# Optimization experiments

Hardware: AMD Instinct MI355X
Metric: run time of the kernel (lower is better)

## Reference

```python
import jax, jax.numpy as jnp
import numpy as np

N = 100_000   # nodes
E = 1_600_000 # edges (avg degree 16)
D_IN = 128
D_H = 128
PROP_STEP = 2


def setup_inputs() -> dict:
    key = jax.random.key(0)
    k = jax.random.split(key, 6)
    in_feat = jax.random.normal(k[0], (N, D_IN), dtype=jnp.float32)
    edge_index = jax.random.randint(k[1], (2, E), 0, N, dtype=jnp.int64)
    s1 = 1.0 / np.sqrt(D_IN)
    s2 = 1.0 / np.sqrt(D_H)
    W1 = jax.random.normal(k[2], (D_IN, D_H), dtype=jnp.float32) * s1
    b1 = jnp.zeros((D_H,), dtype=jnp.float32)
    W2 = jax.random.normal(k[3], (D_H, D_H), dtype=jnp.float32) * s2
    b2 = jnp.zeros((D_H,), dtype=jnp.float32)
    return {"in_feat": in_feat, "edge_index": edge_index,
            "W1": W1, "b1": b1, "W2": W2, "b2": b2}


def _degree_norms(src, dst):
    ones = jnp.ones((src.shape[0],), dtype=jnp.float32)
    deg_out = jax.ops.segment_sum(ones, src, num_segments=N)
    deg_in = jax.ops.segment_sum(ones, dst, num_segments=N)
    # DGL clamps degree to >= 1 before norm='both'
    dout = jnp.maximum(deg_out, 1.0) ** -0.5  # applied to source features
    din = jnp.maximum(deg_in, 1.0) ** -0.5    # applied after aggregation
    return dout, din


def _gcn_conv(x, src, dst, dout, din, W, b):
    # D_in^{-1/2} A D_out^{-1/2} X W + b  (DGL GraphConv, norm='both')
    m = (x * dout[:, None])[src]                      # [E, D] gather
    agg = jax.ops.segment_sum(m, dst, num_segments=N) # [N, D] scatter-add
    return (agg * din[:, None]) @ W + b


def reference(in_feat, edge_index, W1, b1, W2, b2):
    src, dst = edge_index[0], edge_index[1]
    dout, din = _degree_norms(src, dst)
    h = _gcn_conv(in_feat, src, dst, dout, din, W1, b1)
    for _ in range(1, PROP_STEP):
        # relu=False and eval mode -> no relu / dropout
        h = _gcn_conv(h, src, dst, dout, din, W2, b2)
    return h
```

## Files before the change

### kernel.cpp

```cpp
#include <hip/hip_runtime.h>
#include <cstdint>
#include <cstddef>

#define DF 128
#define PB 512
#define RSH 8
#define RNG 256
#define CAP 6144

typedef short bf16x8 __attribute__((ext_vector_type(8)));
typedef float f32x4 __attribute__((ext_vector_type(4)));

__device__ __forceinline__ unsigned short f2b(float f) {
  unsigned u = __builtin_bit_cast(unsigned, f);
  u = (u + 0x7FFFu + ((u >> 16) & 1u)) >> 16;
  return (unsigned short)u;
}
__device__ __forceinline__ float b2f(unsigned short h) {
  return __builtin_bit_cast(float, (unsigned)h << 16);
}
__device__ __forceinline__ unsigned pack2(float lo, float hi) {
  return (unsigned)f2b(lo) | ((unsigned)f2b(hi) << 16);
}

__device__ __forceinline__ int edge_at(const void* ei, long long idx, int is32) {
  return is32 ? ((const int*)ei)[idx] : (int)((const long long*)ei)[idx];
}

__global__ void detect_dtype_kernel(const unsigned* __restrict__ ei, long long nelem,
                                    int* __restrict__ flag) {
  long long half = nelem / 2;
  int t = threadIdx.x + blockIdx.x * blockDim.x;
  long long step = (half + 2047) / 2048;
  long long k = (long long)t * step;
  if (k < half && ei[2 * k + 1] != 0) atomicOr(flag, 1);
}

__global__ __launch_bounds__(256) void part_count_kernel(
    const void* __restrict__ ei, long long E, int nbuck, int chunk,
    int* __restrict__ H, const int* __restrict__ flag) {
  __shared__ int hd[512], hs[512];
  int is32 = *flag;
  int blk = blockIdx.x, t = threadIdx.x;
  for (int i = t; i < 512; i += 256) { hd[i] = 0; hs[i] = 0; }
  __syncthreads();
  long long lo = (long long)blk * chunk;
  long long hi = lo + chunk; if (hi > E) hi = E;
  for (long long e = lo + t; e < hi; e += 256) {
    int s = edge_at(ei, e, is32);
    int d = edge_at(ei, E + e, is32);
    atomicAdd(&hs[s >> RSH], 1);
    atomicAdd(&hd[d >> RSH], 1);
  }
  __syncthreads();
  for (int b = t; b < nbuck; b += 256) {
    H[(size_t)b * PB + blk] = hd[b];
    H[((size_t)nbuck + b) * PB + blk] = hs[b];
  }
}

__device__ __forceinline__ int wave_incl_scan(int v, int lane) {
#pragma unroll
  for (int off = 1; off < 64; off <<= 1) {
    int t = __shfl_up(v, off, 64);
    if (lane >= off) v += t;
  }
  return v;
}

__global__ void chunk_sum_kernel(const int* __restrict__ deg, int* __restrict__ partials, int n) {
  __shared__ int wsum[16];
  int tid = threadIdx.x, lane = tid & 63, wid = tid >> 6;
  int base = blockIdx.x * 4096 + tid * 4;
  int s = 0;
#pragma unroll
  for (int q = 0; q < 4; ++q) { int i = base + q; if (i < n) s += deg[i]; }
#pragma unroll
  for (int off = 32; off; off >>= 1) s += __shfl_down(s, off, 64);
  if (lane == 0) wsum[wid] = s;
  __syncthreads();
  if (tid == 0) {
    int t = 0;
#pragma unroll
    for (int w = 0; w < 16; ++w) t += wsum[w];
    partials[blockIdx.x] = t;
  }
}

__global__ void scan_partials_kernel(int* __restrict__ partials, int nb) {
  int lane = threadIdx.x;
  int carry = 0;
  for (int base = 0; base < nb; base += 64) {
    int i = base + lane;
    int v = (i < nb) ? partials[i] : 0;
    int s = wave_incl_scan(v, lane);
    if (i < nb) partials[i] = s - v + carry;
    carry += __shfl(s, 63, 64);
  }
}

__global__ void scan_chunk_kernel(const int* __restrict__ deg, const int* __restrict__ chunk_off,
                                  int* __restrict__ row_ptr, int n) {
  __shared__ int wsum[16];
  int tid = threadIdx.x, lane = tid & 63, wid = tid >> 6;
  int base = blockIdx.x * 4096 + tid * 4;
  int v0 = (base + 0 < n) ? deg[base + 0] : 0;
  int v1 = (base + 1 < n) ? deg[base + 1] : 0;
  int v2 = (base + 2 < n) ? deg[base + 2] : 0;
  int v3 = (base + 3 < n) ? deg[base + 3] : 0;
  int p0 = v0, p1 = p0 + v1, p2 = p1 + v2, p3 = p2 + v3;
  int ws = wave_incl_scan(p3, lane);
  if (lane == 63) wsum[wid] = ws;
  __syncthreads();
  if (wid == 0) {
    int x = (lane < 16) ? wsum[lane] : 0;
    x = wave_incl_scan(x, lane);
    if (lane < 16) wsum[lane] = x;
  }
  __syncthreads();
  int off = (wid > 0 ? wsum[wid - 1] : 0) + (ws - p3) + chunk_off[blockIdx.x];
  if (base + 0 < n) row_ptr[base + 1] = off + p0;
  if (base + 1 < n) row_ptr[base + 2] = off + p1;
  if (base + 2 < n) row_ptr[base + 3] = off + p2;
  if (base + 3 < n) row_ptr[base + 4] = off + p3;
  if (blockIdx.x == 0 && tid == 0) row_ptr[0] = 0;
}

__global__ __launch_bounds__(256) void part_scatter_kernel(
    const void* __restrict__ ei, long long E, int nbuck, int chunk,
    const int* __restrict__ Hs, unsigned* __restrict__ pack_d,
    unsigned char* __restrict__ src_loc, const int* __restrict__ flag) {
  __shared__ int hd[512], hs[512], bd[512], bs[512];
  int is32 = *flag;
  int blk = blockIdx.x, t = threadIdx.x;
  for (int i = t; i < 512; i += 256) { hd[i] = 0; hs[i] = 0; }
  __syncthreads();
  for (int b = t; b < nbuck; b += 256) {
    bd[b] = Hs[(size_t)b * PB + blk];
    bs[b] = Hs[((size_t)nbuck + b) * PB + blk] - (int)E;
  }
  __syncthreads();
  long long lo = (long long)blk * chunk;
  long long hi = lo + chunk; if (hi > E) hi = E;
  for (long long e = lo + t; e < hi; e += 256) {
    int s = edge_at(ei, e, is32);
    int d = edge_at(ei, E + e, is32);
    int kb = d >> RSH;
    int rd = atomicAdd(&hd[kb], 1);
    pack_d[bd[kb] + rd] = ((unsigned)(d & (RNG - 1)) << 24) | (unsigned)s;
    int ks = s >> RSH;
    int rs = atomicAdd(&hs[ks], 1);
    src_loc[bs[ks] + rs] = (unsigned char)(s & (RNG - 1));
  }
}

__global__ __launch_bounds__(256) void bucket_build_kernel(
    const unsigned* __restrict__ pack_d, const int* __restrict__ Hs,
    long long E, int n, int* __restrict__ row_ptr, float* __restrict__ nin,
    int* __restrict__ csr_src) {
  __shared__ unsigned stage[CAP];
  __shared__ int cnt[RNG], cur[RNG], woff[4];
  int b = blockIdx.x, t = threadIdx.x;
  int lane = t & 63, wv = t >> 6;
  int start = Hs[(size_t)b * PB];
  int end = Hs[(size_t)(b + 1) * PB];
  int len = end - start;
  cnt[t] = 0;
  __syncthreads();
  bool fits = (len <= CAP);
  for (int i = t; i < len; i += 256) {
    unsigned p = pack_d[start + i];
    if (fits) stage[i] = p;
    atomicAdd(&cnt[p >> 24], 1);
  }
  __syncthreads();
  int dreg = cnt[t];
  int isc = wave_incl_scan(dreg, lane);
  if (lane == 63) woff[wv] = isc;
  __syncthreads();
  int add = 0;
#pragma unroll
  for (int w = 0; w < 4; ++w) if (w < wv) add += woff[w];
  int excl = isc - dreg + add;
  int nd = b * RNG + t;
  if (nd < n) {
    row_ptr[nd] = start + excl;
    nin[nd] = rsqrtf((float)(dreg > 1 ? dreg : 1));
  }
  if (b == (int)gridDim.x - 1 && t == 0) row_ptr[n] = (int)E;
  cur[t] = excl;
  __syncthreads();
  for (int i = t; i < len; i += 256) {
    unsigned p = fits ? stage[i] : pack_d[start + i];
    int dl = (int)(p >> 24);
    int r = atomicAdd(&cur[dl], 1);
    csr_src[start + r] = (int)(p & 0xFFFFFFu);
  }
}

__global__ __launch_bounds__(256) void src_deg_kernel(
    const unsigned char* __restrict__ src_loc, const int* __restrict__ Hs,
    int nbuck, long long E, int n, float* __restrict__ nout) {
  __shared__ int cnt[RNG];
  int b = blockIdx.x, t = threadIdx.x;
  int start = Hs[(size_t)(nbuck + b) * PB] - (int)E;
  int end = Hs[(size_t)(nbuck + b + 1) * PB] - (int)E;
  cnt[t] = 0;
  __syncthreads();
  for (int i = start + t; i < end; i += 256) atomicAdd(&cnt[src_loc[i]], 1);
  __syncthreads();
  int nd = b * RNG + t;
  if (nd < n) nout[nd] = rsqrtf((float)(cnt[t] > 1 ? cnt[t] : 1));
}

__global__ __launch_bounds__(256) void prescale_kernel(
    const float* __restrict__ x, const float* __restrict__ nout,
    unsigned short* __restrict__ xh, int n) {
  long long base = ((long long)blockIdx.x * 256 + threadIdx.x) * 8;
  if (base >= (long long)n * DF) return;
  float s = nout[(int)(base >> 7)];
  float4 a = *((const float4*)(x + base));
  float4 b = *((const float4*)(x + base + 4));
  uint4 o;
  o.x = pack2(a.x * s, a.y * s);
  o.y = pack2(a.z * s, a.w * s);
  o.z = pack2(b.x * s, b.y * s);
  o.w = pack2(b.z * s, b.w * s);
  *((uint4*)(xh + base)) = o;
}

__global__ void w_prep_kernel(const float* __restrict__ W1, const float* __restrict__ W2,
                              unsigned short* __restrict__ Wswz) {
  int chunk = blockIdx.x * 256 + threadIdx.x;
  if (chunk >= 8192) return;
  int w = chunk >> 12;
  int rem = chunk & 4095;
  int part = rem >> 11;
  int t = (rem >> 6) & 31;
  int l = rem & 63;
  int jb = t >> 2, ks = t & 3;
  const float* W = w ? W2 : W1;
  int c = jb * 16 + (l & 15);
  int k0 = ks * 32 + ((l >> 4) << 3);
  unsigned v[4];
#pragma unroll
  for (int p = 0; p < 4; ++p) {
    float f0 = W[(size_t)(k0 + 2 * p) * DF + c];
    float f1 = W[(size_t)(k0 + 2 * p + 1) * DF + c];
    unsigned short h0 = f2b(f0), h1 = f2b(f1);
    unsigned short o0 = part ? f2b(f0 - b2f(h0)) : h0;
    unsigned short o1 = part ? f2b(f1 - b2f(h1)) : h1;
    v[p] = (unsigned)o0 | ((unsigned)o1 << 16);
  }
  uint4 o; o.x = v[0]; o.y = v[1]; o.z = v[2]; o.w = v[3];
  ((uint4*)Wswz)[chunk] = o;
}

__global__ __launch_bounds__(256) void aggregate_bf16_kernel(
    const unsigned short* __restrict__ xh, const int* __restrict__ row_ptr,
    const int* __restrict__ csr_src, unsigned short* __restrict__ aggh, int n) {
  int wave = blockIdx.x * (blockDim.x >> 6) + (threadIdx.x >> 6);
  int lane = threadIdx.x & 63;
  if (wave >= n) return;
  int beg = row_ptr[wave], end = row_ptr[wave + 1];
  int deg = end - beg;
  int half = lane >> 5;
  int sub = lane & 31;
  float ax = 0.f, ay = 0.f, az = 0.f, aw = 0.f;
  for (int j0 = 0; j0 < deg; j0 += 64) {
    int li = beg + j0 + lane;
    int idx = csr_src[li < end ? li : (end - 1)];
    int cnt = deg - j0; if (cnt > 64) cnt = 64;
    int tfull = (cnt >> 4) << 3;
    for (int t0 = 0; t0 < tfull; t0 += 8) {
      ushort4 v[8];
#pragma unroll
      for (int u = 0; u < 8; ++u) {
        int s = __shfl(idx, 2 * (t0 + u) + half, 64);
        v[u] = *((const ushort4*)(xh + (size_t)s * DF) + sub);
      }
#pragma unroll
      for (int u = 0; u < 8; ++u) {
        ax += b2f(v[u].x); ay += b2f(v[u].y);
        az += b2f(v[u].z); aw += b2f(v[u].w);
      }
    }
    int cnt2 = (cnt + 1) >> 1;
    for (int t = tfull; t < cnt2; ++t) {
      int p = 2 * t + half;
      int s = __shfl(idx, p, 64);
      float m = (p < cnt) ? 1.f : 0.f;
      ushort4 v = *((const ushort4*)(xh + (size_t)s * DF) + sub);
      ax += b2f(v.x) * m; ay += b2f(v.y) * m;
      az += b2f(v.z) * m; aw += b2f(v.w) * m;
    }
  }
  ax += __shfl_down(ax, 32, 64);
  ay += __shfl_down(ay, 32, 64);
  az += __shfl_down(az, 32, 64);
  aw += __shfl_down(aw, 32, 64);
  if (half == 0) {
    uint2 pk; pk.x = pack2(ax, ay); pk.y = pack2(az, aw);
    *((uint2*)(aggh + (size_t)wave * DF + sub * 4)) = pk;
  }
}

template <int BF16OUT>
__global__ __launch_bounds__(256) void transform_mfma_kernel(
    const unsigned short* __restrict__ aggh, const unsigned short* __restrict__ Wswz,
    const float* __restrict__ nin, const float* __restrict__ bias,
    const float* __restrict__ sc_out, void* __restrict__ outp, int n, int ntiles) {
  __shared__ uint4 Wl[4096];
  int tid = threadIdx.x;
  for (int i = tid; i < 4096; i += 256) Wl[i] = ((const uint4*)Wswz)[i];
  __syncthreads();
  int l = tid & 63, wv = tid >> 6;
  int lr = l & 15, lg = l >> 4;
  for (int tile = blockIdx.x; tile < ntiles; tile += gridDim.x) {
    int rowbase = tile * 64 + wv * 16;
    int r_eff = rowbase + lr; if (r_eff > n - 1) r_eff = n - 1;
    const unsigned short* arow = aggh + (size_t)r_eff * DF + (lg << 3);
    bf16x8 a0 = *(const bf16x8*)(arow);
    bf16x8 a1 = *(const bf16x8*)(arow + 32);
    bf16x8 a2 = *(const bf16x8*)(arow + 64);
    bf16x8 a3 = *(const bf16x8*)(arow + 96);
    f32x4 acc[8];
#pragma unroll
    for (int jb = 0; jb < 8; ++jb) acc[jb] = (f32x4){0.f, 0.f, 0.f, 0.f};
#pragma unroll
    for (int ks = 0; ks < 4; ++ks) {
      bf16x8 a = (ks == 0) ? a0 : (ks == 1) ? a1 : (ks == 2) ? a2 : a3;
#pragma unroll
      for (int jb = 0; jb < 8; ++jb) {
        bf16x8 bh = *(const bf16x8*)&Wl[(jb * 4 + ks) * 64 + l];
        acc[jb] = __builtin_amdgcn_mfma_f32_16x16x32_bf16(a, bh, acc[jb], 0, 0, 0);
        bf16x8 bl = *(const bf16x8*)&Wl[2048 + (jb * 4 + ks) * 64 + l];
        acc[jb] = __builtin_amdgcn_mfma_f32_16x16x32_bf16(a, bl, acc[jb], 0, 0, 0);
      }
    }
    float ninq[4], soq[4];
#pragma unroll
    for (int q = 0; q < 4; ++q) {
      int r = rowbase + lg * 4 + q;
      ninq[q] = (r < n) ? nin[r] : 0.f;
      soq[q] = (r < n) ? (sc_out ? sc_out[r] : 1.f) : 0.f;
    }
#pragma unroll
    for (int jb = 0; jb < 8; ++jb) {
      int c = jb * 16 + lr;
      float bj = bias[c];
#pragma unroll
      for (int q = 0; q < 4; ++q) {
        int r = rowbase + lg * 4 + q;
        if (r < n) {
          float val = (acc[jb][q] * ninq[q] + bj) * soq[q];
          if (BF16OUT) {
            ((unsigned short*)outp)[(size_t)r * DF + c] = f2b(val);
          } else {
            ((float*)outp)[(size_t)r * DF + c] = val;
          }
        }
      }
    }
  }
}

extern "C" void kernel_launch(void* const* d_in, const int* in_sizes, int n_in,
                              void* d_out, int out_size, void* d_ws, size_t ws_size,
                              hipStream_t stream) {
  const float* in_feat = (const float*)d_in[0];
  const void*  ei      = d_in[1];
  const float* W1 = (const float*)d_in[2];
  const float* b1 = (const float*)d_in[3];
  const float* W2 = (const float*)d_in[4];
  const float* b2 = (const float*)d_in[5];
  float* out = (float*)d_out;

  const int N = in_sizes[0] / DF;
  const long long E = in_sizes[1] / 2;
  const int nbuck = (N + RNG - 1) >> RSH;
  const int M = 2 * nbuck * PB;
  const int NB2 = (M + 4095) / 4096;
  const int chunk = (int)((E + PB - 1) / PB);
  const int ntiles = (N + 63) / 64;

  size_t off = 0;
  auto take = [&](size_t nb) -> char* {
    char* p = (char*)d_ws + off;
    off += (nb + 255) & ~(size_t)255;
    return p;
  };
  int* H          = (int*)take((size_t)M * 4);
  int* Hs         = (int*)take((size_t)(M + 1) * 4);
  int* partials   = (int*)take((size_t)NB2 * 4);
  int* row_ptr    = (int*)take((size_t)(N + 1) * 4);
  float* nout     = (float*)take((size_t)N * 4);
  float* nin      = (float*)take((size_t)N * 4);
  int* flag       = (int*)take(4);
  unsigned* pack_d = (unsigned*)take((size_t)E * 4);
  unsigned char* src_loc = (unsigned char*)take((size_t)E);
  int* csr_src    = (int*)take((size_t)E * 4);
  unsigned short* x1h = (unsigned short*)take((size_t)N * DF * 2);
  unsigned short* h1h = (unsigned short*)take((size_t)N * DF * 2);
  unsigned short* aggh = (unsigned short*)take((size_t)N * DF * 2);
  unsigned short* Wswz = (unsigned short*)take(2 * 65536);
  (void)ws_size; (void)n_in; (void)out_size;

  hipMemsetAsync(flag, 0, 4, stream);
  detect_dtype_kernel<<<8, 256, 0, stream>>>((const unsigned*)ei, (long long)in_sizes[1], flag);

  part_count_kernel<<<PB, 256, 0, stream>>>(ei, E, nbuck, chunk, H, flag);
  chunk_sum_kernel<<<NB2, 1024, 0, stream>>>(H, partials, M);
  scan_partials_kernel<<<1, 64, 0, stream>>>(partials, NB2);
  scan_chunk_kernel<<<NB2, 1024, 0, stream>>>(H, partials, Hs, M);
  part_scatter_kernel<<<PB, 256, 0, stream>>>(ei, E, nbuck, chunk, Hs, pack_d, src_loc, flag);
  bucket_build_kernel<<<nbuck, 256, 0, stream>>>(pack_d, Hs, E, N, row_ptr, nin, csr_src);
  src_deg_kernel<<<nbuck, 256, 0, stream>>>(src_loc, Hs, nbuck, E, N, nout);

  w_prep_kernel<<<32, 256, 0, stream>>>(W1, W2, Wswz);

  int pb = (int)(((long long)N * DF / 8 + 255) / 256);
  prescale_kernel<<<pb, 256, 0, stream>>>(in_feat, nout, x1h, N);

  int ab = (N + 3) / 4;
  aggregate_bf16_kernel<<<ab, 256, 0, stream>>>(x1h, row_ptr, csr_src, aggh, N);
  transform_mfma_kernel<1><<<512, 256, 0, stream>>>(aggh, Wswz, nin, b1, nout, h1h, N, ntiles);
  aggregate_bf16_kernel<<<ab, 256, 0, stream>>>(h1h, row_ptr, csr_src, aggh, N);
  transform_mfma_kernel<0><<<512, 256, 0, stream>>>(aggh, Wswz + 32768, nin, b2, nullptr, out, N, ntiles);
}
```

Measured before the change: 313.1 us.

## Fuse aggregation with MFMA transform via per-wave LDS stripes and dynamic scheduling

Merges the gather/scatter aggregation and the MFMA linear transform into one persistent kernel. Each wave atomically grabs 16-node chunks, aggregates them into an LDS stripe and applies the weight matmul directly, so the intermediate aggregation buffer never goes through global memory. Also folds dtype detection into the partition kernels and source-degree counting into bucket_build, removing several launches. The trade-offs are a 512-block persistent grid with one wave per chunk, which may lower the memory-level parallelism of the gather, plus extra LDS pressure from the stripes alongside the weight tile.

Result: slower. 512.8 us (+63.8%).

```diff
diff --git a/kernel.cpp b/kernel.cpp
--- a/kernel.cpp
+++ b/kernel.cpp
@@ -27,25 +27,29 @@
   return is32 ? ((const int*)ei)[idx] : (int)((const long long*)ei)[idx];
 }
 
-__global__ void detect_dtype_kernel(const unsigned* __restrict__ ei, long long nelem,
-                                    int* __restrict__ flag) {
-  long long half = nelem / 2;
-  int t = threadIdx.x + blockIdx.x * blockDim.x;
-  long long step = (half + 2047) / 2048;
-  long long k = (long long)t * step;
-  if (k < half && ei[2 * k + 1] != 0) atomicOr(flag, 1);
+__device__ __forceinline__ int detect_is32(const void* ei, long long lo, long long hi,
+                                           int* s_flag) {
+  int t = threadIdx.x;
+  if (t == 0) *s_flag = 0;
+  __syncthreads();
+  int bad = 0;
+  long long cap = lo + 2048; if (cap > hi) cap = hi;
+  for (long long e = lo + t; e < cap; e += 256)
+    bad |= (((const unsigned*)ei)[2 * e + 1] != 0);
+  if (bad) atomicOr(s_flag, 1);
+  __syncthreads();
+  return *s_flag;
 }
 
 __global__ __launch_bounds__(256) void part_count_kernel(
     const void* __restrict__ ei, long long E, int nbuck, int chunk,
-    int* __restrict__ H, const int* __restrict__ flag) {
-  __shared__ int hd[512], hs[512];
-  int is32 = *flag;
+    int* __restrict__ H) {
+  __shared__ int hd[512], hs[512], s_flag;
   int blk = blockIdx.x, t = threadIdx.x;
   for (int i = t; i < 512; i += 256) { hd[i] = 0; hs[i] = 0; }
-  __syncthreads();
   long long lo = (long long)blk * chunk;
   long long hi = lo + chunk; if (hi > E) hi = E;
+  int is32 = detect_is32(ei, lo, hi, &s_flag);
   for (long long e = lo + t; e < hi; e += 256) {
     int s = edge_at(ei, e, is32);
     int d = edge_at(ei, E + e, is32);
@@ -129,19 +133,18 @@
 __global__ __launch_bounds__(256) void part_scatter_kernel(
     const void* __restrict__ ei, long long E, int nbuck, int chunk,
     const int* __restrict__ Hs, unsigned* __restrict__ pack_d,
-    unsigned char* __restrict__ src_loc, const int* __restrict__ flag) {
+    unsigned char* __restrict__ src_loc) {
   __shared__ int hd[512], hs[512], bd[512], bs[512];
-  int is32 = *flag;
+  __shared__ int s_flag;
   int blk = blockIdx.x, t = threadIdx.x;
   for (int i = t; i < 512; i += 256) { hd[i] = 0; hs[i] = 0; }
-  __syncthreads();
   for (int b = t; b < nbuck; b += 256) {
     bd[b] = Hs[(size_t)b * PB + blk];
     bs[b] = Hs[((size_t)nbuck + b) * PB + blk] - (int)E;
   }
-  __syncthreads();
   long long lo = (long long)blk * chunk;
   long long hi = lo + chunk; if (hi > E) hi = E;
+  int is32 = detect_is32(ei, lo, hi, &s_flag);
   for (long long e = lo + t; e < hi; e += 256) {
     int s = edge_at(ei, e, is32);
     int d = edge_at(ei, E + e, is32);
@@ -155,8 +158,9 @@
 }
 
 __global__ __launch_bounds__(256) void bucket_build_kernel(
-    const unsigned* __restrict__ pack_d, const int* __restrict__ Hs,
-    long long E, int n, int* __restrict__ row_ptr, float* __restrict__ nin,
+    const unsigned* __restrict__ pack_d, const unsigned char* __restrict__ src_loc,
+    const int* __restrict__ Hs, int nbuck, long long E, int n,
+    int* __restrict__ row_ptr, float* __restrict__ nin, float* __restrict__ nout,
     int* __restrict__ csr_src) {
   __shared__ unsigned stage[CAP];
   __shared__ int cnt[RNG], cur[RNG], woff[4];
@@ -196,20 +200,13 @@
     int r = atomicAdd(&cur[dl], 1);
     csr_src[start + r] = (int)(p & 0xFFFFFFu);
   }
-}
-
-__global__ __launch_bounds__(256) void src_deg_kernel(
-    const unsigned char* __restrict__ src_loc, const int* __restrict__ Hs,
-    int nbuck, long long E, int n, float* __restrict__ nout) {
-  __shared__ int cnt[RNG];
-  int b = blockIdx.x, t = threadIdx.x;
-  int start = Hs[(size_t)(nbuck + b) * PB] - (int)E;
-  int end = Hs[(size_t)(nbuck + b + 1) * PB] - (int)E;
+  __syncthreads();
   cnt[t] = 0;
   __syncthreads();
-  for (int i = start + t; i < end; i += 256) atomicAdd(&cnt[src_loc[i]], 1);
-  __syncthreads();
-  int nd = b * RNG + t;
+  int sstart = Hs[(size_t)(nbuck + b) * PB] - (int)E;
+  int send = Hs[(size_t)(nbuck + b + 1) * PB] - (int)E;
+  for (int i = sstart + t; i < send; i += 256) atomicAdd(&cnt[src_loc[i]], 1);
+  __syncthreads();
   if (nd < n) nout[nd] = rsqrtf((float)(cnt[t] > 1 ? cnt[t] : 1));
 }
 
@@ -256,74 +253,76 @@
   ((uint4*)Wswz)[chunk] = o;
 }
 
-__global__ __launch_bounds__(256) void aggregate_bf16_kernel(
+template <int BF16OUT>
+__global__ __launch_bounds__(256) void fused_conv_kernel(
     const unsigned short* __restrict__ xh, const int* __restrict__ row_ptr,
-    const int* __restrict__ csr_src, unsigned short* __restrict__ aggh, int n) {
-  int wave = blockIdx.x * (blockDim.x >> 6) + (threadIdx.x >> 6);
-  int lane = threadIdx.x & 63;
-  if (wave >= n) return;
-  int beg = row_ptr[wave], end = row_ptr[wave + 1];
-  int deg = end - beg;
-  int half = lane >> 5;
-  int sub = lane & 31;
-  float ax = 0.f, ay = 0.f, az = 0.f, aw = 0.f;
-  for (int j0 = 0; j0 < deg; j0 += 64) {
-    int li = beg + j0 + lane;
-    int idx = csr_src[li < end ? li : (end - 1)];
-    int cnt = deg - j0; if (cnt > 64) cnt = 64;
-    int tfull = (cnt >> 4) << 3;
-    for (int t0 = 0; t0 < tfull; t0 += 8) {
-      ushort4 v[8];
-#pragma unroll
-      for (int u = 0; u < 8; ++u) {
-        int s = __shfl(idx, 2 * (t0 + u) + half, 64);
-        v[u] = *((const ushort4*)(xh + (size_t)s * DF) + sub);
+    const int* __restrict__ csr_src, const unsigned short* __restrict__ Wswz,
+    const float* __restrict__ nin, const float* __restrict__ bias,
+    const float* __restrict__ sc_out, void* __restrict__ outp, int n,
+    int nchunks, int* __restrict__ ctr) {
+  __shared__ uint4 Wl[4096];
+  __shared__ unsigned short stripe[4][2048];
+  int tid = threadIdx.x;
+  for (int i = tid; i < 4096; i += 256) Wl[i] = ((const uint4*)Wswz)[i];
+  __syncthreads();
+  int l = tid & 63, wv = tid >> 6;
+  int half = l >> 5, sub = l & 31;
+  int lr = l & 15, lg = l >> 4;
+  unsigned short* st = stripe[wv];
+  for (;;) {
+    int chunk = 0;
+    if (l == 0) chunk = atomicAdd(ctr, 1);
+    chunk = __shfl(chunk, 0, 64);
+    if (chunk >= nchunks) break;
+    int base = chunk * 16;
+    for (int j = 0; j < 16; ++j) {
+      int node = base + j;
+      float ax = 0.f, ay = 0.f, az = 0.f, aw = 0.f;
+      if (node < n) {
+        int beg = row_ptr[node], end = row_ptr[node + 1];
+        int deg = end - beg;
+        for (int j0 = 0; j0 < deg; j0 += 64) {
+          int li = beg + j0 + l;
+          int idx = csr_src[li < end ? li : (end - 1)];
+          int cnt = deg - j0; if (cnt > 64) cnt = 64;
+          int tfull = (cnt >> 4) << 3;
+          for (int t0 = 0; t0 < tfull; t0 += 8) {
+            ushort4 v[8];
+#pragma unroll
+            for (int u = 0; u < 8; ++u) {
+              int s = __shfl(idx, 2 * (t0 + u) + half, 64);
+              v[u] = *((const ushort4*)(xh + (size_t)s * DF) + sub);
+            }
+#pragma unroll
+            for (int u = 0; u < 8; ++u) {
+              ax += b2f(v[u].x); ay += b2f(v[u].y);
+              az += b2f(v[u].z); aw += b2f(v[u].w);
+            }
+          }
+          int cnt2 = (cnt + 1) >> 1;
+          for (int t = tfull; t < cnt2; ++t) {
+            int p = 2 * t + half;
+            int s = __shfl(idx, p, 64);
+            float m = (p < cnt) ? 1.f : 0.f;
+            ushort4 v = *((const ushort4*)(xh + (size_t)s * DF) + sub);
+            ax += b2f(v.x) * m; ay += b2f(v.y) * m;
+            az += b2f(v.z) * m; aw += b2f(v.w) * m;
+          }
+        }
       }
-#pragma unroll
-      for (int u = 0; u < 8; ++u) {
-        ax += b2f(v[u].x); ay += b2f(v[u].y);
-        az += b2f(v[u].z); aw += b2f(v[u].w);
+      ax += __shfl_down(ax, 32, 64);
+      ay += __shfl_down(ay, 32, 64);
+      az += __shfl_down(az, 32, 64);
+      aw += __shfl_down(aw, 32, 64);
+      if (half == 0) {
+        uint2 pk; pk.x = pack2(ax, ay); pk.y = pack2(az, aw);
+        *((uint2*)(st + j * 128 + sub * 4)) = pk;
       }
     }
-    int cnt2 = (cnt + 1) >> 1;
-    for (int t = tfull; t < cnt2; ++t) {
-      int p = 2 * t + half;
-      int s = __shfl(idx, p, 64);
-      float m = (p < cnt) ? 1.f : 0.f;
-      ushort4 v = *((const ushort4*)(xh + (size_t)s * DF) + sub);
-      ax += b2f(v.x) * m; ay += b2f(v.y) * m;
-      az += b2f(v.z) * m; aw += b2f(v.w) * m;
-    }
-  }
-  ax += __shfl_down(ax, 32, 64);
-  ay += __shfl_down(ay, 32, 64);
-  az += __shfl_down(az, 32, 64);
-  aw += __shfl_down(aw, 32, 64);
-  if (half == 0) {
-    uint2 pk; pk.x = pack2(ax, ay); pk.y = pack2(az, aw);
-    *((uint2*)(aggh + (size_t)wave * DF + sub * 4)) = pk;
-  }
-}
-
-template <int BF16OUT>
-__global__ __launch_bounds__(256) void transform_mfma_kernel(
-    const unsigned short* __restrict__ aggh, const unsigned short* __restrict__ Wswz,
-    const float* __restrict__ nin, const float* __restrict__ bias,
-    const float* __restrict__ sc_out, void* __restrict__ outp, int n, int ntiles) {
-  __shared__ uint4 Wl[4096];
-  int tid = threadIdx.x;
-  for (int i = tid; i < 4096; i += 256) Wl[i] = ((const uint4*)Wswz)[i];
-  __syncthreads();
-  int l = tid & 63, wv = tid >> 6;
-  int lr = l & 15, lg = l >> 4;
-  for (int tile = blockIdx.x; tile < ntiles; tile += gridDim.x) {
-    int rowbase = tile * 64 + wv * 16;
-    int r_eff = rowbase + lr; if (r_eff > n - 1) r_eff = n - 1;
-    const unsigned short* arow = aggh + (size_t)r_eff * DF + (lg << 3);
-    bf16x8 a0 = *(const bf16x8*)(arow);
-    bf16x8 a1 = *(const bf16x8*)(arow + 32);
-    bf16x8 a2 = *(const bf16x8*)(arow + 64);
-    bf16x8 a3 = *(const bf16x8*)(arow + 96);
+    bf16x8 a0 = *(const bf16x8*)(st + lr * 128 + 0 * 32 + lg * 8);
+    bf16x8 a1 = *(const bf16x8*)(st + lr * 128 + 1 * 32 + lg * 8);
+    bf16x8 a2 = *(const bf16x8*)(st + lr * 128 + 2 * 32 + lg * 8);
+    bf16x8 a3 = *(const bf16x8*)(st + lr * 128 + 3 * 32 + lg * 8);
     f32x4 acc[8];
 #pragma unroll
     for (int jb = 0; jb < 8; ++jb) acc[jb] = (f32x4){0.f, 0.f, 0.f, 0.f};
@@ -341,7 +340,7 @@
     float ninq[4], soq[4];
 #pragma unroll
     for (int q = 0; q < 4; ++q) {
-      int r = rowbase + lg * 4 + q;
+      int r = base + lg * 4 + q;
       ninq[q] = (r < n) ? nin[r] : 0.f;
       soq[q] = (r < n) ? (sc_out ? sc_out[r] : 1.f) : 0.f;
     }
@@ -351,7 +350,7 @@
       float bj = bias[c];
 #pragma unroll
       for (int q = 0; q < 4; ++q) {
-        int r = rowbase + lg * 4 + q;
+        int r = base + lg * 4 + q;
         if (r < n) {
           float val = (acc[jb][q] * ninq[q] + bj) * soq[q];
           if (BF16OUT) {
@@ -382,7 +381,7 @@
   const int M = 2 * nbuck * PB;
   const int NB2 = (M + 4095) / 4096;
   const int chunk = (int)((E + PB - 1) / PB);
-  const int ntiles = (N + 63) / 64;
+  const int nchunks = (N + 15) / 16;
 
   size_t off = 0;
   auto take = [&](size_t nb) -> char* {
@@ -396,35 +395,32 @@
   int* row_ptr    = (int*)take((size_t)(N + 1) * 4);
   float* nout     = (float*)take((size_t)N * 4);
   float* nin      = (float*)take((size_t)N * 4);
-  int* flag       = (int*)take(4);
+  int* ctr        = (int*)take(8);
   unsigned* pack_d = (unsigned*)take((size_t)E * 4);
   unsigned char* src_loc = (unsigned char*)take((size_t)E);
   int* csr_src    = (int*)take((size_t)E * 4);
   unsigned short* x1h = (unsigned short*)take((size_t)N * DF * 2);
   unsigned short* h1h = (unsigned short*)take((size_t)N * DF * 2);
-  unsigned short* aggh = (unsigned short*)take((size_t)N * DF * 2);
   unsigned short* Wswz = (unsigned short*)take(2 * 65536);
   (void)ws_size; (void)n_in; (void)out_size;
 
-  hipMemsetAsync(flag, 0, 4, stream);
-  detect_dtype_kernel<<<8, 256, 0, stream>>>((const unsigned*)ei, (long long)in_sizes[1], flag);
-
-  part_count_kernel<<<PB, 256, 0, stream>>>(ei, E, nbuck, chunk, H, flag);
+  hipMemsetAsync(ctr, 0, 8, stream);
+
+  part_count_kernel<<<PB, 256, 0, stream>>>(ei, E, nbuck, chunk, H);
   chunk_sum_kernel<<<NB2, 1024, 0, stream>>>(H, partials, M);
   scan_partials_kernel<<<1, 64, 0, stream>>>(partials, NB2);
   scan_chunk_kernel<<<NB2, 1024, 0, stream>>>(H, partials, Hs, M);
-  part_scatter_kernel<<<PB, 256, 0, stream>>>(ei, E, nbuck, chunk, Hs, pack_d, src_loc, flag);
-  bucket_build_kernel<<<nbuck, 256, 0, stream>>>(pack_d, Hs, E, N, row_ptr, nin, csr_src);
-  src_deg_kernel<<<nbuck, 256, 0, stream>>>(src_loc, Hs, nbuck, E, N, nout);
+  part_scatter_kernel<<<PB, 256, 0, stream>>>(ei, E, nbuck, chunk, Hs, pack_d, src_loc);
+  bucket_build_kernel<<<nbuck, 256, 0, stream>>>(pack_d, src_loc, Hs, nbuck, E, N,
+                                                 row_ptr, nin, nout, csr_src);
 
   w_prep_kernel<<<32, 256, 0, stream>>>(W1, W2, Wswz);
 
   int pb = (int)(((long long)N * DF / 8 + 255) / 256);
   prescale_kernel<<<pb, 256, 0, stream>>>(in_feat, nout, x1h, N);
 
-  int ab = (N + 3) / 4;
-  aggregate_bf16_kernel<<<ab, 256, 0, stream>>>(x1h, row_ptr, csr_src, aggh, N);
-  transform_mfma_kernel<1><<<512, 256, 0, stream>>>(aggh, Wswz, nin, b1, nout, h1h, N, ntiles);
-  aggregate_bf16_kernel<<<ab, 256, 0, stream>>>(h1h, row_ptr, csr_src, aggh, N);
-  transform_mfma_kernel<0><<<512, 256, 0, stream>>>(aggh, Wswz + 32768, nin, b2, nullptr, out, N, ntiles);
-}
+  fused_conv_kernel<1><<<512, 256, 0, stream>>>(x1h, row_ptr, csr_src, Wswz,
+                                                nin, b1, nout, h1h, N, nchunks, ctr);
+  fused_conv_kernel<0><<<512, 256, 0, stream>>>(h1h, row_ptr, csr_src, Wswz + 32768,
+                                                nin, b2, nullptr, out, N, nchunks, ctr + 1);
+}
```

## Fuse dtype detection, source-degree and prescale into partition/bucket kernels

Applied to the files above, without the earlier changes.

Removes the separate dtype-detection kernel and memset by having each partition block check its own edge chunk for 64-bit indices. It also folds the source-degree count and the input prescale-to-bf16 into bucket_build_kernel, dropping two launches and one re-read of nout. The cost is that per-block dtype detection is local to each chunk, so blocks could disagree on the dtype. The fused kernel also does more serial work per block across only nbuck blocks, which limits parallelism for the prescale.

Result: faster. 305.4 us (-2.5%).

```diff
diff --git a/kernel.cpp b/kernel.cpp
--- a/kernel.cpp
+++ b/kernel.cpp
@@ -27,25 +27,29 @@
   return is32 ? ((const int*)ei)[idx] : (int)((const long long*)ei)[idx];
 }
 
-__global__ void detect_dtype_kernel(const unsigned* __restrict__ ei, long long nelem,
-                                    int* __restrict__ flag) {
-  long long half = nelem / 2;
-  int t = threadIdx.x + blockIdx.x * blockDim.x;
-  long long step = (half + 2047) / 2048;
-  long long k = (long long)t * step;
-  if (k < half && ei[2 * k + 1] != 0) atomicOr(flag, 1);
+__device__ __forceinline__ int detect_is32(const void* ei, long long lo, long long hi,
+                                           int* s_flag) {
+  int t = threadIdx.x;
+  if (t == 0) *s_flag = 0;
+  __syncthreads();
+  int bad = 0;
+  long long cap = lo + 2048; if (cap > hi) cap = hi;
+  for (long long e = lo + t; e < cap; e += 256)
+    bad |= (((const unsigned*)ei)[2 * e + 1] != 0);
+  if (bad) atomicOr(s_flag, 1);
+  __syncthreads();
+  return *s_flag;
 }
 
 __global__ __launch_bounds__(256) void part_count_kernel(
     const void* __restrict__ ei, long long E, int nbuck, int chunk,
-    int* __restrict__ H, const int* __restrict__ flag) {
-  __shared__ int hd[512], hs[512];
-  int is32 = *flag;
+    int* __restrict__ H) {
+  __shared__ int hd[512], hs[512], s_flag;
   int blk = blockIdx.x, t = threadIdx.x;
   for (int i = t; i < 512; i += 256) { hd[i] = 0; hs[i] = 0; }
-  __syncthreads();
   long long lo = (long long)blk * chunk;
   long long hi = lo + chunk; if (hi > E) hi = E;
+  int is32 = detect_is32(ei, lo, hi, &s_flag);
   for (long long e = lo + t; e < hi; e += 256) {
     int s = edge_at(ei, e, is32);
     int d = edge_at(ei, E + e, is32);
@@ -129,19 +133,18 @@
 __global__ __launch_bounds__(256) void part_scatter_kernel(
     const void* __restrict__ ei, long long E, int nbuck, int chunk,
     const int* __restrict__ Hs, unsigned* __restrict__ pack_d,
-    unsigned char* __restrict__ src_loc, const int* __restrict__ flag) {
+    unsigned char* __restrict__ src_loc) {
   __shared__ int hd[512], hs[512], bd[512], bs[512];
-  int is32 = *flag;
+  __shared__ int s_flag;
   int blk = blockIdx.x, t = threadIdx.x;
   for (int i = t; i < 512; i += 256) { hd[i] = 0; hs[i] = 0; }
-  __syncthreads();
   for (int b = t; b < nbuck; b += 256) {
     bd[b] = Hs[(size_t)b * PB + blk];
     bs[b] = Hs[((size_t)nbuck + b) * PB + blk] - (int)E;
   }
-  __syncthreads();
   long long lo = (long long)blk * chunk;
   long long hi = lo + chunk; if (hi > E) hi = E;
+  int is32 = detect_is32(ei, lo, hi, &s_flag);
   for (long long e = lo + t; e < hi; e += 256) {
     int s = edge_at(ei, e, is32);
     int d = edge_at(ei, E + e, is32);
@@ -155,11 +158,14 @@
 }
 
 __global__ __launch_bounds__(256) void bucket_build_kernel(
-    const unsigned* __restrict__ pack_d, const int* __restrict__ Hs,
-    long long E, int n, int* __restrict__ row_ptr, float* __restrict__ nin,
-    int* __restrict__ csr_src) {
+    const unsigned* __restrict__ pack_d, const unsigned char* __restrict__ src_loc,
+    const int* __restrict__ Hs, int nbuck, long long E, int n,
+    int* __restrict__ row_ptr, float* __restrict__ nin, float* __restrict__ nout,
+    int* __restrict__ csr_src,
+    const float* __restrict__ in_feat, unsigned short* __restrict__ x1h) {
   __shared__ unsigned stage[CAP];
   __shared__ int cnt[RNG], cur[RNG], woff[4];
+  __shared__ float fn[RNG];
   int b = blockIdx.x, t = threadIdx.x;
   int lane = t & 63, wv = t >> 6;
   int start = Hs[(size_t)b * PB];
@@ -196,37 +202,32 @@
     int r = atomicAdd(&cur[dl], 1);
     csr_src[start + r] = (int)(p & 0xFFFFFFu);
   }
-}
-
-__global__ __launch_bounds__(256) void src_deg_kernel(
-    const unsigned char* __restrict__ src_loc, const int* __restrict__ Hs,
-    int nbuck, long long E, int n, float* __restrict__ nout) {
-  __shared__ int cnt[RNG];
-  int b = blockIdx.x, t = threadIdx.x;
-  int start = Hs[(size_t)(nbuck + b) * PB] - (int)E;
-  int end = Hs[(size_t)(nbuck + b + 1) * PB] - (int)E;
+  __syncthreads();
   cnt[t] = 0;
   __syncthreads();
-  for (int i = start + t; i < end; i += 256) atomicAdd(&cnt[src_loc[i]], 1);
-  __syncthreads();
-  int nd = b * RNG + t;
-  if (nd < n) nout[nd] = rsqrtf((float)(cnt[t] > 1 ? cnt[t] : 1));
-}
-
-__global__ __launch_bounds__(256) void prescale_kernel(
-    const float* __restrict__ x, const float* __restrict__ nout,
-    unsigned short* __restrict__ xh, int n) {
-  long long base = ((long long)blockIdx.x * 256 + threadIdx.x) * 8;
-  if (base >= (long long)n * DF) return;
-  float s = nout[(int)(base >> 7)];
-  float4 a = *((const float4*)(x + base));
-  float4 b = *((const float4*)(x + base + 4));
-  uint4 o;
-  o.x = pack2(a.x * s, a.y * s);
-  o.y = pack2(a.z * s, a.w * s);
-  o.z = pack2(b.x * s, b.y * s);
-  o.w = pack2(b.z * s, b.w * s);
-  *((uint4*)(xh + base)) = o;
+  int sstart = Hs[(size_t)(nbuck + b) * PB] - (int)E;
+  int send = Hs[(size_t)(nbuck + b + 1) * PB] - (int)E;
+  for (int i = sstart + t; i < send; i += 256) atomicAdd(&cnt[src_loc[i]], 1);
+  __syncthreads();
+  float nv = rsqrtf((float)(cnt[t] > 1 ? cnt[t] : 1));
+  fn[t] = nv;
+  if (nd < n) nout[nd] = nv;
+  __syncthreads();
+  for (int c = t; c < RNG * DF / 8; c += 256) {
+    int jl = c >> 4;
+    int node = b * RNG + jl;
+    if (node >= n) break;
+    float s = fn[jl];
+    long long base = (long long)node * DF + (c & 15) * 8;
+    float4 a = *((const float4*)(in_feat + base));
+    float4 bb = *((const float4*)(in_feat + base + 4));
+    uint4 o;
+    o.x = pack2(a.x * s, a.y * s);
+    o.y = pack2(a.z * s, a.w * s);
+    o.z = pack2(bb.x * s, bb.y * s);
+    o.w = pack2(bb.z * s, bb.w * s);
+    *((uint4*)(x1h + base)) = o;
+  }
 }
 
 __global__ void w_prep_kernel(const float* __restrict__ W1, const float* __restrict__ W2,
@@ -396,7 +397,6 @@
   int* row_ptr    = (int*)take((size_t)(N + 1) * 4);
   float* nout     = (float*)take((size_t)N * 4);
   float* nin      = (float*)take((size_t)N * 4);
-  int* flag       = (int*)take(4);
   unsigned* pack_d = (unsigned*)take((size_t)E * 4);
   unsigned char* src_loc = (unsigned char*)take((size_t)E);
   int* csr_src    = (int*)take((size_t)E * 4);
@@ -406,21 +406,15 @@
   unsigned short* Wswz = (unsigned short*)take(2 * 65536);
   (void)ws_size; (void)n_in; (void)out_size;
 
-  hipMemsetAsync(flag, 0, 4, stream);
-  detect_dtype_kernel<<<8, 256, 0, stream>>>((const unsigned*)ei, (long long)in_sizes[1], flag);
-
-  part_count_kernel<<<PB, 256, 0, stream>>>(ei, E, nbuck, chunk, H, flag);
+  part_count_kernel<<<PB, 256, 0, stream>>>(ei, E, nbuck, chunk, H);
   chunk_sum_kernel<<<NB2, 1024, 0, stream>>>(H, partials, M);
   scan_partials_kernel<<<1, 64, 0, stream>>>(partials, NB2);
   scan_chunk_kernel<<<NB2, 1024, 0, stream>>>(H, partials, Hs, M);
-  part_scatter_kernel<<<PB, 256, 0, stream>>>(ei, E, nbuck, chunk, Hs, pack_d, src_loc, flag);
-  bucket_build_kernel<<<nbuck, 256, 0, stream>>>(pack_d, Hs, E, N, row_ptr, nin, csr_src);
-  src_deg_kernel<<<nbuck, 256, 0, stream>>>(src_loc, Hs, nbuck, E, N, nout);
-
+  part_scatter_kernel<<<PB, 256, 0, stream>>>(ei, E, nbuck, chunk, Hs, pack_d, src_loc);
+  bucket_build_kernel<<<nbuck, 256, 0, stream>>>(pack_d, src_loc, Hs, nbuck, E, N,
+                                                 row_ptr, nin, nout, csr_src,
+                                                 in_feat, x1h);
   w_prep_kernel<<<32, 256, 0, stream>>>(W1, W2, Wswz);
-
-  int pb = (int)(((long long)N * DF / 8 + 255) / 256);
-  prescale_kernel<<<pb, 256, 0, stream>>>(in_feat, nout, x1h, N);
 
   int ab = (N + 3) / 4;
   aggregate_bf16_kernel<<<ab, 256, 0, stream>>>(x1h, row_ptr, csr_src, aggh, N);
```
